# Kernel optimization log

Measured on AMD Instinct MI355X. Metric: run time of the kernel, lower is better.

Reference implementation:

```python
import jax, jax.numpy as jnp
import numpy as np

N_NODES = 100000
N_EDGES = 1600000
EPS = 1e-12


def setup_inputs() -> dict:
    key = jax.random.key(0)
    ks = jax.random.split(key, 8)
    features = jax.random.normal(ks[0], (N_NODES, 128), dtype=jnp.float32)
    src = jax.random.randint(ks[1], (N_EDGES,), 0, N_NODES, dtype=jnp.int64)
    dst = jax.random.randint(ks[2], (N_EDGES,), 0, N_NODES, dtype=jnp.int64)
    w1 = jax.random.normal(ks[3], (32, 128), dtype=jnp.float32) * 0.05
    b1 = jax.random.normal(ks[4], (32,), dtype=jnp.float32) * 0.05
    betas = jnp.ones((2,), dtype=jnp.float32)  # AGNNConv init_beta=1.0, one per layer
    w2 = jax.random.normal(ks[5], (64, 32), dtype=jnp.float32) * 0.05
    b2 = jax.random.normal(ks[6], (64,), dtype=jnp.float32) * 0.05
    return {"features": features, "src": src, "dst": dst,
            "w1": w1, "b1": b1, "betas": betas, "w2": w2, "b2": b2}


def _agnn_conv(h, src, dst, beta):
    # cosine similarity on normalized features, per edge (src -> dst)
    hn = h / jnp.maximum(jnp.linalg.norm(h, axis=1, keepdims=True), EPS)
    e = beta * jnp.sum(hn[src] * hn[dst], axis=1)  # [E]
    # edge softmax grouped by destination node (stable)
    m = jax.ops.segment_max(e, dst, num_segments=N_NODES)
    m = jnp.where(jnp.isfinite(m), m, 0.0)  # zero-in-degree guard
    ex = jnp.exp(e - m[dst])
    denom = jax.ops.segment_sum(ex, dst, num_segments=N_NODES)
    alpha = ex / jnp.maximum(denom[dst], EPS)
    # attention-weighted scatter-sum of (unnormalized) source features
    return jax.ops.segment_sum(alpha[:, None] * h[src], dst, num_segments=N_NODES)


def reference(features, src, dst, w1, b1, betas, w2, b2):
    h = jax.nn.relu(features @ w1.T + b1)
    for i in range(betas.shape[0]):
        h = jax.nn.relu(_agnn_conv(h, src, dst, betas[i]))
    out = h @ w2.T + b2
    return jax.nn.log_softmax(out, axis=1)
```

## Files before the change

kernel.cpp:

```cpp
#include <hip/hip_runtime.h>
#include <hip/hip_fp16.h>

#define NNODES 100000
#define NEDGES 1600000

#define BSHIFT 7
#define BSIZE  128
#define NBUCK  ((NNODES + BSIZE - 1) >> BSHIFT)
#define SSEG   32
#define BIN_EPT  16
#define BIN_TILE (256 * BIN_EPT)
#define NBINBLK  ((NEDGES + BIN_TILE - 1) / BIN_TILE)

#define GBLK  (NNODES / 32)

static_assert(NNODES % 32 == 0, "agnn assumes exact 32-node blocks");

static constexpr float EPS = 1e-12f;
static constexpr float LOG2E = 1.44269504f;

__device__ __forceinline__ float2 h2f(unsigned u) {
    __half2 h = __builtin_bit_cast(__half2, u);
    return __half22float2(h);
}

#if defined(__has_builtin)
#if __has_builtin(__builtin_amdgcn_fdot2)
#define HAVE_FDOT2 1
#endif
#if __has_builtin(__builtin_amdgcn_exp2f)
#define EXP2F(x) __builtin_amdgcn_exp2f(x)
#endif
#endif
#ifndef EXP2F
#define EXP2F(x) __expf((x) * 0.69314718f)
#endif

#define FMAMIX_LO(acc, pk, s) \
    asm("v_fma_mix_f32 %0, %1, %2, %0 op_sel:[0,0,0] op_sel_hi:[1,0,0]" \
        : "+v"(acc) : "v"(pk), "v"(s))
#define FMAMIX_HI(acc, pk, s) \
    asm("v_fma_mix_f32 %0, %1, %2, %0 op_sel:[1,0,0] op_sel_hi:[1,0,0]" \
        : "+v"(acc) : "v"(pk), "v"(s))

__device__ __forceinline__ float fdot2p(unsigned a, unsigned b, float c) {
#ifdef HAVE_FDOT2
    typedef _Float16 h2v __attribute__((ext_vector_type(2)));
    return __builtin_amdgcn_fdot2(__builtin_bit_cast(h2v, a),
                                  __builtin_bit_cast(h2v, b), c, false);
#else
    float2 fa = h2f(a), fb = h2f(b);
    return c + fa.x * fb.x + fa.y * fb.y;
#endif
}
__device__ __forceinline__ float dot16(uint4 a, uint4 b) {
    return fdot2p(a.x, b.x, fdot2p(a.y, b.y, fdot2p(a.z, b.z,
           fdot2p(a.w, b.w, 0.f))));
}

template <int CTRL>
__device__ __forceinline__ float dppadd(float x) {
    int y = __builtin_amdgcn_update_dpp(0, __builtin_bit_cast(int, x),
                                        CTRL, 0xF, 0xF, true);
    return x + __builtin_bit_cast(float, y);
}
template <int CTRL>
__device__ __forceinline__ float dppmax(float x) {
    int y = __builtin_amdgcn_update_dpp(0, __builtin_bit_cast(int, x),
                                        CTRL, 0xF, 0xF, true);
    return fmaxf(x, __builtin_bit_cast(float, y));
}
__device__ __forceinline__ float swz4add(float x) {
    int y = __builtin_amdgcn_ds_swizzle(__builtin_bit_cast(int, x), 0x101F);
    return x + __builtin_bit_cast(float, y);
}
__device__ __forceinline__ float swz16add(float x) {
    int y = __builtin_amdgcn_ds_swizzle(__builtin_bit_cast(int, x), 0x401F);
    return x + __builtin_bit_cast(float, y);
}
__device__ __forceinline__ float swz16max(float x) {
    int y = __builtin_amdgcn_ds_swizzle(__builtin_bit_cast(int, x), 0x401F);
    return fmaxf(x, __builtin_bit_cast(float, y));
}
__device__ __forceinline__ float red4(float x) {
    x = dppadd<0xB1>(x);
    x = dppadd<0x4E>(x);
    return x;
}
__device__ __forceinline__ float red64(float x) {
    x = dppadd<0xB1>(x); x = dppadd<0x4E>(x);
    x = dppadd<0x141>(x); x = dppadd<0x128>(x);
    x = swz16add(x);
    x += __shfl_xor(x, 32);
    return x;
}
__device__ __forceinline__ float red64max(float x) {
    x = dppmax<0xB1>(x); x = dppmax<0x4E>(x);
    x = dppmax<0x141>(x); x = dppmax<0x128>(x);
    x = swz16max(x);
    x = fmaxf(x, __shfl_xor(x, 32));
    return x;
}


__global__ __launch_bounds__(256) void k_bhist(
    const int* __restrict__ dst, int* __restrict__ bcnt)
{
    __shared__ int cnt[NBUCK];
    for (int i = threadIdx.x; i < NBUCK; i += 256) cnt[i] = 0;
    __syncthreads();
    int base = blockIdx.x * BIN_TILE;
    #pragma unroll
    for (int i = 0; i < BIN_EPT; ++i) {
        int k = base + i * 256 + threadIdx.x;
        if (k < NEDGES) atomicAdd(&cnt[dst[k] >> BSHIFT], 1);
    }
    __syncthreads();
    for (int i = threadIdx.x; i < NBUCK; i += 256)
        if (cnt[i]) atomicAdd(&bcnt[i], cnt[i]);
}

__global__ __launch_bounds__(256) void k_bscan(
    const int* __restrict__ bcnt, int* __restrict__ bbase,
    int* __restrict__ bcur, int* __restrict__ rowptr)
{
    const int CH = (NBUCK + 255) / 256;
    __shared__ int ls[256];
    int t = threadIdx.x;
    int base = t * CH;
    int s = 0;
    #pragma unroll
    for (int i = 0; i < CH; ++i) {
        int idx = base + i;
        if (idx < NBUCK) s += bcnt[idx];
    }
    ls[t] = s;
    __syncthreads();
    for (int off = 1; off < 256; off <<= 1) {
        int u = (t >= off) ? ls[t - off] : 0;
        __syncthreads();
        ls[t] += u;
        __syncthreads();
    }
    int run = (t == 0) ? 0 : ls[t - 1];
    #pragma unroll
    for (int i = 0; i < CH; ++i) {
        int idx = base + i;
        if (idx < NBUCK) {
            bbase[idx] = run;
            bcur[idx]  = run;
            run += bcnt[idx];
        }
    }
    if (t == 0) rowptr[NNODES] = NEDGES;
}

__global__ __launch_bounds__(256) void k_bin(
    const int* __restrict__ src, const int* __restrict__ dst,
    int* __restrict__ bcur, unsigned* __restrict__ packed)
{
    __shared__ int cnt[NBUCK];
    __shared__ int gb[NBUCK];
    for (int i = threadIdx.x; i < NBUCK; i += 256) cnt[i] = 0;
    __syncthreads();
    unsigned pk[BIN_EPT];
    int bk[BIN_EPT];
    int base = blockIdx.x * BIN_TILE;
    #pragma unroll
    for (int i = 0; i < BIN_EPT; ++i) {
        int k = base + i * 256 + threadIdx.x;
        bk[i] = -1;
        if (k < NEDGES) {
            int d = dst[k], s = src[k];
            bk[i] = d >> BSHIFT;
            pk[i] = ((unsigned)(d & (BSIZE - 1)) << 17) | (unsigned)s;
            atomicAdd(&cnt[bk[i]], 1);
        }
    }
    __syncthreads();
    for (int i = threadIdx.x; i < NBUCK; i += 256) {
        int c = cnt[i];
        gb[i] = c ? atomicAdd(&bcur[i], c) : 0;
        cnt[i] = 0;
    }
    __syncthreads();
    #pragma unroll
    for (int i = 0; i < BIN_EPT; ++i) {
        if (bk[i] >= 0) {
            int pos = gb[bk[i]] + atomicAdd(&cnt[bk[i]], 1);
            packed[pos] = pk[i];
        }
    }
}

__global__ __launch_bounds__(256) void k_bucket(
    const unsigned* __restrict__ packed, const int* __restrict__ bbase,
    const int* __restrict__ bcnt, int* __restrict__ rowptr,
    int* __restrict__ esrc)
{
    __shared__ int cnt[BSIZE * SSEG];
    __shared__ int ls[256];
    int b = blockIdx.x, t = threadIdx.x;
    int base = bbase[b], n = bcnt[b];
    for (int i = t; i < BSIZE * SSEG; i += 256) cnt[i] = 0;
    __syncthreads();
    for (int i = t; i < n; i += 256) {
        unsigned p = packed[base + i];
        int key = (int)(p >> 17) * SSEG + (int)((p & 0x1FFFFu) >> 12);
        atomicAdd(&cnt[key], 1);
    }
    __syncthreads();
    const int CH = BSIZE * SSEG / 256;
    int base_k = t * CH;
    int vals[CH];
    int s = 0;
    #pragma unroll
    for (int i = 0; i < CH; ++i) { vals[i] = cnt[base_k + i]; s += vals[i]; }
    ls[t] = s;
    __syncthreads();
    for (int off = 1; off < 256; off <<= 1) {
        int u = (t >= off) ? ls[t - off] : 0;
        __syncthreads();
        ls[t] += u;
        __syncthreads();
    }
    int run = base + ((t == 0) ? 0 : ls[t - 1]);
    #pragma unroll
    for (int i = 0; i < CH; ++i) {
        int key = base_k + i;
        if ((key & (SSEG - 1)) == 0) {
            int node = b * BSIZE + (key / SSEG);
            if (node < NNODES) rowptr[node] = run;
        }
        cnt[key] = run;
        run += vals[i];
    }
    __syncthreads();
    for (int i = t; i < n; i += 256) {
        unsigned p = packed[base + i];
        int key = (int)(p >> 17) * SSEG + (int)((p & 0x1FFFFu) >> 12);
        int pos = atomicAdd(&cnt[key], 1);
        esrc[pos] = (int)(p & 0x1FFFFu);
    }
}


__global__ __launch_bounds__(256) void k_lin1(
    const float* __restrict__ feat, const float* __restrict__ w1,
    const float* __restrict__ b1, __half* __restrict__ hn16,
    float* __restrict__ nrm)
{
    __shared__ float4 w1s[32][32];
    int t = threadIdx.x;
    {
        const float4* w4 = reinterpret_cast<const float4*>(w1);
        float4* ws = &w1s[0][0];
        #pragma unroll
        for (int i = 0; i < 4; ++i) ws[t + i * 256] = w4[t + i * 256];
    }
    __syncthreads();

    int row = blockIdx.x * 256 + t;
    if (row >= NNODES) return;

    const float4* fr = reinterpret_cast<const float4*>(feat + (size_t)row * 128);
    float4 f[32];
    #pragma unroll
    for (int k = 0; k < 32; ++k) f[k] = fr[k];

    float acc[32];
    #pragma unroll
    for (int c = 0; c < 32; ++c) acc[c] = b1[c];

    #pragma unroll
    for (int k = 0; k < 32; ++k) {
        #pragma unroll
        for (int c = 0; c < 32; ++c) {
            float4 w = w1s[c][k];
            acc[c] = fmaf(f[k].x, w.x, acc[c]);
            acc[c] = fmaf(f[k].y, w.y, acc[c]);
            acc[c] = fmaf(f[k].z, w.z, acc[c]);
            acc[c] = fmaf(f[k].w, w.w, acc[c]);
        }
    }

    float ss = 0.f;
    #pragma unroll
    for (int c = 0; c < 32; ++c) {
        acc[c] = fmaxf(acc[c], 0.f);
        ss = fmaf(acc[c], acc[c], ss);
    }
    float n = fmaxf(sqrtf(ss), EPS);
    float rn = 1.f / n;
    unsigned q[16];
    #pragma unroll
    for (int j = 0; j < 16; ++j) {
        __half2 hh = __floats2half2_rn(acc[2 * j] * rn, acc[2 * j + 1] * rn);
        q[j] = __builtin_bit_cast(unsigned, hh);
    }
    uint4* o4 = reinterpret_cast<uint4*>(hn16 + (size_t)row * 32);
    o4[0] = make_uint4(q[0],  q[1],  q[2],  q[3]);
    o4[1] = make_uint4(q[4],  q[5],  q[6],  q[7]);
    o4[2] = make_uint4(q[8],  q[9],  q[10], q[11]);
    o4[3] = make_uint4(q[12], q[13], q[14], q[15]);
    nrm[row] = n;
}

template <bool FUSED>
__global__ __launch_bounds__(256) void k_agnn(
    const __half* __restrict__ hn16, const float* __restrict__ nrm,
    const int* __restrict__ rowptr, const int* __restrict__ esrc,
    const float* __restrict__ betas, int layer,
    __half* __restrict__ hnout, float* __restrict__ nout,
    const float* __restrict__ w2, const float* __restrict__ b2,
    float* __restrict__ out)
{
    __shared__ float w2s[FUSED ? 64 : 1][33];
    __shared__ float osm[FUSED ? 32 : 1][33];
    int t = threadIdx.x;
    if constexpr (FUSED) {
        for (int i = t; i < 64 * 32; i += 256)
            w2s[i >> 5][i & 31] = w2[i];
        __syncthreads();
    }
    int wid  = t >> 6;
    int lane = t & 63;
    int grp  = lane >> 2;
    int pair = grp >> 1;
    int half = grp & 1;
    int c4   = lane & 3;

    int node = blockIdx.x * 32 + wid * 8 + pair;
    int start = rowptr[node], end = rowptr[node + 1];

    const uint4* hrow = reinterpret_cast<const uint4*>(hn16);
    float beta = betas[layer];
    float bl2 = beta * LOG2E;
    float cl2 = -fabsf(beta) * LOG2E;
    uint4 qd = hrow[(size_t)node * 4 + c4];

    float den = 0.f;
    float acc[8] = {0.f, 0.f, 0.f, 0.f, 0.f, 0.f, 0.f, 0.f};

    for (int i = start + 4 * half; i < end; i += 8) {
        int rem = end - i;
        int s0 = esrc[i];
        int s1 = (rem > 1) ? esrc[i + 1] : s0;
        int s2 = (rem > 2) ? esrc[i + 2] : s0;
        int s3 = (rem > 3) ? esrc[i + 3] : s0;
        uint4 q0 = hrow[(size_t)s0 * 4 + c4];
        uint4 q1 = hrow[(size_t)s1 * 4 + c4];
        uint4 q2 = hrow[(size_t)s2 * 4 + c4];
        uint4 q3 = hrow[(size_t)s3 * 4 + c4];
        float n0 = nrm[s0], n1 = nrm[s1], n2 = nrm[s2], n3 = nrm[s3];
        float p0 = red4(dot16(q0, qd));
        float p1 = red4(dot16(q1, qd));
        float p2 = red4(dot16(q2, qd));
        float p3 = red4(dot16(q3, qd));
        float w0 = EXP2F(fmaf(bl2, p0, cl2));
        float w1 = (rem > 1) ? EXP2F(fmaf(bl2, p1, cl2)) : 0.f;
        float w2v = (rem > 2) ? EXP2F(fmaf(bl2, p2, cl2)) : 0.f;
        float w3 = (rem > 3) ? EXP2F(fmaf(bl2, p3, cl2)) : 0.f;
        float wn0 = w0 * n0, wn1 = w1 * n1, wn2 = w2v * n2, wn3 = w3 * n3;
        den += (w0 + w1) + (w2v + w3);
        FMAMIX_LO(acc[0], q0.x, wn0); FMAMIX_HI(acc[1], q0.x, wn0);
        FMAMIX_LO(acc[2], q0.y, wn0); FMAMIX_HI(acc[3], q0.y, wn0);
        FMAMIX_LO(acc[4], q0.z, wn0); FMAMIX_HI(acc[5], q0.z, wn0);
        FMAMIX_LO(acc[6], q0.w, wn0); FMAMIX_HI(acc[7], q0.w, wn0);
        FMAMIX_LO(acc[0], q1.x, wn1); FMAMIX_HI(acc[1], q1.x, wn1);
        FMAMIX_LO(acc[2], q1.y, wn1); FMAMIX_HI(acc[3], q1.y, wn1);
        FMAMIX_LO(acc[4], q1.z, wn1); FMAMIX_HI(acc[5], q1.z, wn1);
        FMAMIX_LO(acc[6], q1.w, wn1); FMAMIX_HI(acc[7], q1.w, wn1);
        FMAMIX_LO(acc[0], q2.x, wn2); FMAMIX_HI(acc[1], q2.x, wn2);
        FMAMIX_LO(acc[2], q2.y, wn2); FMAMIX_HI(acc[3], q2.y, wn2);
        FMAMIX_LO(acc[4], q2.z, wn2); FMAMIX_HI(acc[5], q2.z, wn2);
        FMAMIX_LO(acc[6], q2.w, wn2); FMAMIX_HI(acc[7], q2.w, wn2);
        FMAMIX_LO(acc[0], q3.x, wn3); FMAMIX_HI(acc[1], q3.x, wn3);
        FMAMIX_LO(acc[2], q3.y, wn3); FMAMIX_HI(acc[3], q3.y, wn3);
        FMAMIX_LO(acc[4], q3.z, wn3); FMAMIX_HI(acc[5], q3.z, wn3);
        FMAMIX_LO(acc[6], q3.w, wn3); FMAMIX_HI(acc[7], q3.w, wn3);
    }

    den = dppadd<0x141>(den);
    #pragma unroll
    for (int j = 0; j < 8; ++j) acc[j] = swz4add(acc[j]);

    float inv = 1.f / fmaxf(den, EPS);
    float o[8];
    #pragma unroll
    for (int j = 0; j < 8; ++j) o[j] = fmaxf(acc[j] * inv, 0.f);

    if constexpr (!FUSED) {
        float ss = 0.f;
        #pragma unroll
        for (int j = 0; j < 8; ++j) ss = fmaf(o[j], o[j], ss);
        ss = red4(ss);
        float nn = fmaxf(sqrtf(ss), EPS);
        float rn = 1.f / nn;
        unsigned q[4];
        #pragma unroll
        for (int j = 0; j < 4; ++j) {
            __half2 hh = __floats2half2_rn(o[2 * j] * rn, o[2 * j + 1] * rn);
            q[j] = __builtin_bit_cast(unsigned, hh);
        }
        if (half == 0) {
            reinterpret_cast<uint4*>(hnout)[(size_t)node * 4 + c4] =
                make_uint4(q[0], q[1], q[2], q[3]);
            if (c4 == 0) nout[node] = nn;
        }
    } else {
        int ls = wid * 8 + pair;
        if (half == 0) {
            float* orow = &osm[ls][c4 * 8];
            #pragma unroll
            for (int j = 0; j < 8; ++j) orow[j] = o[j];
        }
        float w2r[32];
        #pragma unroll
        for (int k = 0; k < 32; ++k) w2r[k] = w2s[lane][k];
        float b2l = b2[lane];
        __syncthreads();
        int nbase = blockIdx.x * 32 + wid * 8;
        #pragma unroll
        for (int p = 0; p < 8; ++p) {
            const float* op = osm[wid * 8 + p];
            float a2 = b2l;
            #pragma unroll
            for (int k = 0; k < 32; ++k) a2 += op[k] * w2r[k];
            float mx = red64max(a2);
            float sm = red64(__expf(a2 - mx));
            out[(size_t)(nbase + p) * 64 + lane] = a2 - mx - __logf(sm);
        }
    }
}

extern "C" void kernel_launch(void* const* d_in, const int* in_sizes, int n_in,
                              void* d_out, int out_size, void* d_ws, size_t ws_size,
                              hipStream_t stream)
{
    const float* feat  = (const float*)d_in[0];
    const int*   src   = (const int*)d_in[1];
    const int*   dst   = (const int*)d_in[2];
    const float* w1    = (const float*)d_in[3];
    const float* b1    = (const float*)d_in[4];
    const float* betas = (const float*)d_in[5];
    const float* w2    = (const float*)d_in[6];
    const float* b2    = (const float*)d_in[7];
    float* out = (float*)d_out;

    __half*   hnA    = (__half*)d_ws;
    __half*   hnB    = hnA + (size_t)NNODES * 32;
    float*    nA     = (float*)(hnB + (size_t)NNODES * 32);
    float*    nB     = nA + NNODES;
    int*      rowptr = (int*)(nB + NNODES);
    int*      esrc   = rowptr + NNODES + 1;
    unsigned* packed = (unsigned*)(esrc + NEDGES);
    int*      bcnt   = (int*)(packed + NEDGES);
    int*      bbase  = bcnt + NBUCK;
    int*      bcur   = bbase + NBUCK;

    dim3 blk(256);
    int gNode = (NNODES + 255) / 256;

    hipMemsetAsync(bcnt, 0, NBUCK * sizeof(int), stream);
    k_bhist<<<NBINBLK, blk, 0, stream>>>(dst, bcnt);
    k_bscan<<<1, blk, 0, stream>>>(bcnt, bbase, bcur, rowptr);
    k_bin<<<NBINBLK, blk, 0, stream>>>(src, dst, bcur, packed);
    k_bucket<<<NBUCK, blk, 0, stream>>>(packed, bbase, bcnt, rowptr, esrc);

    k_lin1<<<gNode, blk, 0, stream>>>(feat, w1, b1, hnA, nA);

    k_agnn<false><<<GBLK, blk, 0, stream>>>(hnA, nA, rowptr, esrc,
                                            betas, 0, hnB, nB,
                                            nullptr, nullptr, nullptr);
    k_agnn<true><<<GBLK, blk, 0, stream>>>(hnB, nB, rowptr, esrc,
                                           betas, 1, nullptr, nullptr,
                                           w2, b2, out);
}
```

Baseline: 166.9 us.

## Use larger 512-node buckets and drop src sub-sorting in CSR build

Widens the coarse destination buckets from 128 to 512 nodes, so there are about 196 buckets, and simplifies the single-block bucket scan to one bucket per thread. The per-bucket CSR kernel now runs 512 threads, one per node, and drops the secondary sort by source segment. Within each row, edges are now in arbitrary atomic order instead of roughly grouped by source. The histogram kernel also uses smaller tiles and more blocks. Fewer, larger buckets make CSR construction cheaper, but the lost source locality may hurt gather cache behavior in the AGNN layers, and there is less block parallelism in k_bucket.

```diff
diff --git a/kernel.cpp b/kernel.cpp
--- a/kernel.cpp
+++ b/kernel.cpp
@@ -4,10 +4,12 @@
 #define NNODES 100000
 #define NEDGES 1600000
 
-#define BSHIFT 7
-#define BSIZE  128
+#define BSHIFT 9
+#define BSIZE  512
 #define NBUCK  ((NNODES + BSIZE - 1) >> BSHIFT)
-#define SSEG   32
+#define HIST_EPT  4
+#define HIST_TILE (256 * HIST_EPT)
+#define NHISTBLK  ((NEDGES + HIST_TILE - 1) / HIST_TILE)
 #define BIN_EPT  16
 #define BIN_TILE (256 * BIN_EPT)
 #define NBINBLK  ((NEDGES + BIN_TILE - 1) / BIN_TILE)
@@ -109,9 +111,9 @@
     __shared__ int cnt[NBUCK];
     for (int i = threadIdx.x; i < NBUCK; i += 256) cnt[i] = 0;
     __syncthreads();
-    int base = blockIdx.x * BIN_TILE;
-    #pragma unroll
-    for (int i = 0; i < BIN_EPT; ++i) {
+    int base = blockIdx.x * HIST_TILE;
+    #pragma unroll
+    for (int i = 0; i < HIST_EPT; ++i) {
         int k = base + i * 256 + threadIdx.x;
         if (k < NEDGES) atomicAdd(&cnt[dst[k] >> BSHIFT], 1);
     }
@@ -124,17 +126,9 @@
     const int* __restrict__ bcnt, int* __restrict__ bbase,
     int* __restrict__ bcur, int* __restrict__ rowptr)
 {
-    const int CH = (NBUCK + 255) / 256;
     __shared__ int ls[256];
     int t = threadIdx.x;
-    int base = t * CH;
-    int s = 0;
-    #pragma unroll
-    for (int i = 0; i < CH; ++i) {
-        int idx = base + i;
-        if (idx < NBUCK) s += bcnt[idx];
-    }
-    ls[t] = s;
+    ls[t] = (t < NBUCK) ? bcnt[t] : 0;
     __syncthreads();
     for (int off = 1; off < 256; off <<= 1) {
         int u = (t >= off) ? ls[t - off] : 0;
@@ -142,15 +136,10 @@
         ls[t] += u;
         __syncthreads();
     }
-    int run = (t == 0) ? 0 : ls[t - 1];
-    #pragma unroll
-    for (int i = 0; i < CH; ++i) {
-        int idx = base + i;
-        if (idx < NBUCK) {
-            bbase[idx] = run;
-            bcur[idx]  = run;
-            run += bcnt[idx];
-        }
+    if (t < NBUCK) {
+        int b = (t == 0) ? 0 : ls[t - 1];
+        bbase[t] = b;
+        bcur[t]  = b;
     }
     if (t == 0) rowptr[NNODES] = NEDGES;
 }
@@ -193,53 +182,38 @@
     }
 }
 
-__global__ __launch_bounds__(256) void k_bucket(
+__global__ __launch_bounds__(512) void k_bucket(
     const unsigned* __restrict__ packed, const int* __restrict__ bbase,
     const int* __restrict__ bcnt, int* __restrict__ rowptr,
     int* __restrict__ esrc)
 {
-    __shared__ int cnt[BSIZE * SSEG];
-    __shared__ int ls[256];
+    __shared__ int cnt[BSIZE];
+    __shared__ int loc[BSIZE];
     int b = blockIdx.x, t = threadIdx.x;
-    int base = bbase[b], n = bcnt[b];
-    for (int i = t; i < BSIZE * SSEG; i += 256) cnt[i] = 0;
-    __syncthreads();
-    for (int i = t; i < n; i += 256) {
+    int base = bbase[b];
+    int n = bcnt[b];
+    cnt[t] = 0;
+    __syncthreads();
+    for (int i = t; i < n; i += 512)
+        atomicAdd(&cnt[packed[base + i] >> 17], 1);
+    __syncthreads();
+    int v = cnt[t];
+    loc[t] = v;
+    __syncthreads();
+    for (int off = 1; off < 512; off <<= 1) {
+        int u = (t >= off) ? loc[t - off] : 0;
+        __syncthreads();
+        loc[t] += u;
+        __syncthreads();
+    }
+    int excl = loc[t] - v;
+    int node = b * BSIZE + t;
+    if (node < NNODES) rowptr[node] = base + excl;
+    cnt[t] = base + excl;
+    __syncthreads();
+    for (int i = t; i < n; i += 512) {
         unsigned p = packed[base + i];
-        int key = (int)(p >> 17) * SSEG + (int)((p & 0x1FFFFu) >> 12);
-        atomicAdd(&cnt[key], 1);
-    }
-    __syncthreads();
-    const int CH = BSIZE * SSEG / 256;
-    int base_k = t * CH;
-    int vals[CH];
-    int s = 0;
-    #pragma unroll
-    for (int i = 0; i < CH; ++i) { vals[i] = cnt[base_k + i]; s += vals[i]; }
-    ls[t] = s;
-    __syncthreads();
-    for (int off = 1; off < 256; off <<= 1) {
-        int u = (t >= off) ? ls[t - off] : 0;
-        __syncthreads();
-        ls[t] += u;
-        __syncthreads();
-    }
-    int run = base + ((t == 0) ? 0 : ls[t - 1]);
-    #pragma unroll
-    for (int i = 0; i < CH; ++i) {
-        int key = base_k + i;
-        if ((key & (SSEG - 1)) == 0) {
-            int node = b * BSIZE + (key / SSEG);
-            if (node < NNODES) rowptr[node] = run;
-        }
-        cnt[key] = run;
-        run += vals[i];
-    }
-    __syncthreads();
-    for (int i = t; i < n; i += 256) {
-        unsigned p = packed[base + i];
-        int key = (int)(p >> 17) * SSEG + (int)((p & 0x1FFFFu) >> 12);
-        int pos = atomicAdd(&cnt[key], 1);
+        int pos = atomicAdd(&cnt[p >> 17], 1);
         esrc[pos] = (int)(p & 0x1FFFFu);
     }
 }
@@ -463,10 +437,10 @@
     int gNode = (NNODES + 255) / 256;
 
     hipMemsetAsync(bcnt, 0, NBUCK * sizeof(int), stream);
-    k_bhist<<<NBINBLK, blk, 0, stream>>>(dst, bcnt);
+    k_bhist<<<NHISTBLK, blk, 0, stream>>>(dst, bcnt);
     k_bscan<<<1, blk, 0, stream>>>(bcnt, bbase, bcur, rowptr);
     k_bin<<<NBINBLK, blk, 0, stream>>>(src, dst, bcur, packed);
-    k_bucket<<<NBUCK, blk, 0, stream>>>(packed, bbase, bcnt, rowptr, esrc);
+    k_bucket<<<NBUCK, 512, 0, stream>>>(packed, bbase, bcnt, rowptr, esrc);
 
     k_lin1<<<gNode, blk, 0, stream>>>(feat, w1, b1, hnA, nA);
 
```

New measurement: 192.4 us. +15.3%, slower.
